# Performance work log

Hardware: AMD Instinct MI355X
Metric: run time of the kernel (lower is better)

Reference implementation:

```python
import jax, jax.numpy as jnp
import numpy as np

N_SITES = 128
BOND = 64
PHYS = 2
BATCH = 8192
EPS = 1e-30


def setup_inputs() -> dict:
    key = jax.random.key(0)
    k0, k1, k2, k3 = jax.random.split(key, 4)
    std = 1.0 / np.sqrt(BOND)  # default init_std in _normal_init
    return {
        "configurations": jax.random.randint(k0, (BATCH, N_SITES), 0, PHYS),
        "left_tensor": jax.random.normal(k1, (1, PHYS, BOND), jnp.float32) * std,
        "bulk_tensors": jax.random.normal(k2, (N_SITES - 2, BOND, PHYS, BOND), jnp.float32) * std,
        "right_tensor": jax.random.normal(k3, (BOND, PHYS, 1), jnp.float32) * std,
    }


def _log_amplitude_squared(left, bulk, right, configs):
    # left: (1,P,D), bulk: (N-2,D,P,D), right: (D,P,1), configs: (B,N) int
    env = left[0, configs[:, 0], :]                         # (B, D)
    m = jnp.clip(jnp.max(jnp.abs(env), axis=1), EPS, None)  # (B,)
    env = env / m[:, None]
    log_scale = jnp.log(m)

    def step(carry, xs):
        env, ls = carry
        A, v = xs                                # A: (D,P,D), v: (B,)
        sel = A[:, v, :]                         # (D, B, D) gathered matrices
        env = jnp.einsum('bi,ibj->bj', env, sel)  # (B, D) batched matvec
        m = jnp.clip(jnp.max(jnp.abs(env), axis=1), EPS, None)
        env = env / m[:, None]
        return (env, ls + jnp.log(m)), None

    (env, log_scale), _ = jax.lax.scan(
        step, (env, log_scale), (bulk, configs[:, 1:-1].T))

    sel = right[:, configs[:, -1], 0]            # (D, B)
    psi = jnp.einsum('bd,db->b', env, sel)       # (B,) rescaled amplitude
    m = jnp.clip(jnp.abs(psi), EPS, None)
    psi = psi / m
    log_scale = log_scale + jnp.log(m)

    abs2 = jnp.clip(psi * psi, EPS, None)
    return jnp.log(abs2) + 2.0 * log_scale      # (B,) log|Psi(v)|^2


def reference(configurations, left_tensor, bulk_tensors, right_tensor):
    return _log_amplitude_squared(left_tensor, bulk_tensors, right_tensor, configurations)
```

## Files before the change

### kernel.cpp

```cpp
#include <hip/hip_runtime.h>
#include <math.h>
#include <stdint.h>

typedef __attribute__((ext_vector_type(8))) short bf16x8;
typedef __attribute__((ext_vector_type(4))) float f32x4;
typedef __attribute__((ext_vector_type(4))) int   i32x4;
typedef __attribute__((ext_vector_type(2))) int   i32x2;

#define NSITES 128
#define NBULK  126
#define BOND   64
#define BATCH  8192

#define WSITE     49152
#define WMASK_OFF ((size_t)NBULK * (size_t)WSITE)
#define WS_NEED   (WMASK_OFF + (size_t)BATCH * 16)

#define EBUF_SZ 12288
#define RED_OFF 24576
#define SMEM_SZ 25088

#define MFMA_BF16 __builtin_amdgcn_mfma_f32_16x16x32_bf16

__global__ void prep_w(const float* __restrict__ bulk, char* __restrict__ wsd) {
    const int s  = blockIdx.x;
    const int t  = threadIdx.x;
    const int jt = (t >> 6) & 3;
    const int l  = t & 63;
    const int j  = jt * 16 + (l & 15);
    const int kb0 = (l >> 4) * 8;
    const float* bs = bulk + (size_t)s * 8192;
    char* dsite = wsd + (size_t)s * WSITE;
    #pragma unroll
    for (int ks = 0; ks < 2; ++ks) {
        const int kb = ks * 32 + kb0;
        #pragma unroll
        for (int v = 0; v < 2; ++v) {
            uint h[3][8];
            #pragma unroll
            for (int e = 0; e < 8; ++e) {
                const float x = bs[(size_t)(kb + e) * 128 + v * 64 + j];
                const uint  u1 = __float_as_uint(x) & 0xffff0000u;
                const float r1 = x - __uint_as_float(u1);
                const uint  u2 = __float_as_uint(r1) & 0xffff0000u;
                const float r2 = r1 - __uint_as_float(u2);
                h[0][e] = u1; h[1][e] = u2;
                h[2][e] = __float_as_uint(r2) & 0xffff0000u;
            }
            #pragma unroll
            for (int tm = 0; tm < 3; ++tm) {
                i32x4 q;
                q.x = (int)((h[tm][0] >> 16) | (h[tm][1] & 0xffff0000u));
                q.y = (int)((h[tm][2] >> 16) | (h[tm][3] & 0xffff0000u));
                q.z = (int)((h[tm][4] >> 16) | (h[tm][5] & 0xffff0000u));
                q.w = (int)((h[tm][6] >> 16) | (h[tm][7] & 0xffff0000u));
                *(i32x4*)(dsite + ((((v*3+tm)*2+ks)*4 + jt) * 1024) + l * 16) = q;
            }
        }
    }
}

__global__ void prep_mask(const int* __restrict__ cfg, uint* __restrict__ msk) {
    const int w = threadIdx.x >> 6, l = threadIdx.x & 63;
    const int b = blockIdx.x * 2 + (w >> 1);
    const int half = w & 1;
    int idx = half * 64 + l + 1;
    if (idx > 127) idx = 127;
    const int v = cfg[b * NSITES + idx];
    const unsigned long long bal = __ballot(v != 0);
    if (l == 0) {
        msk[b * 4 + half * 2]     = (uint)(bal & 0xffffffffu);
        msk[b * 4 + half * 2 + 1] = (uint)(bal >> 32);
    }
}


#define PREFETCH_A(S, DBUF) do { \
    if ((S) < NBULK) { \
        const char* gp_ = ws + (size_t)(S) * WSITE; \
        _Pragma("unroll") for (int vv = 0; vv < 2; ++vv) \
        _Pragma("unroll") for (int tm = 0; tm < 3; ++tm) \
        _Pragma("unroll") for (int ks = 0; ks < 2; ++ks) \
            Areg[DBUF][vv][tm][ks] = *(const bf16x8*)(gp_ + aG[vv][tm][ks]); \
    } \
} while (0)

#define PUBLISH(PW) do { \
    uint pa_[3][4]; \
    _Pragma("unroll") \
    for (int r = 0; r < 4; ++r) { \
        const float x_ = eg0[r]; \
        const uint  u1_ = __float_as_uint(x_) & 0xffff0000u; \
        const float r1_ = x_ - __uint_as_float(u1_); \
        const uint  u2_ = __float_as_uint(r1_) & 0xffff0000u; \
        const float r2_ = r1_ - __uint_as_float(u2_); \
        pa_[0][r] = u1_; pa_[1][r] = u2_; \
        pa_[2][r] = __float_as_uint(r2_) & 0xffff0000u; \
    } \
    _Pragma("unroll") \
    for (int tm = 0; tm < 3; ++tm) { \
        i32x2 d_; \
        d_.x = (int)((pa_[tm][0] >> 16) | (pa_[tm][1] & 0xffff0000u)); \
        d_.y = (int)((pa_[tm][2] >> 16) | (pa_[tm][3] & 0xffff0000u)); \
        *(i32x2*)(smem + aW[PW] + tm * 2048) = d_; \
    } \
    _Pragma("unroll") \
    for (int r = 0; r < 4; ++r) { \
        const float x_ = eg1[r]; \
        const uint  u1_ = __float_as_uint(x_) & 0xffff0000u; \
        const float r1_ = x_ - __uint_as_float(u1_); \
        const uint  u2_ = __float_as_uint(r1_) & 0xffff0000u; \
        const float r2_ = r1_ - __uint_as_float(u2_); \
        pa_[0][r] = u1_; pa_[1][r] = u2_; \
        pa_[2][r] = __float_as_uint(r2_) & 0xffff0000u; \
    } \
    _Pragma("unroll") \
    for (int tm = 0; tm < 3; ++tm) { \
        i32x2 d_; \
        d_.x = (int)((pa_[tm][0] >> 16) | (pa_[tm][1] & 0xffff0000u)); \
        d_.y = (int)((pa_[tm][2] >> 16) | (pa_[tm][3] & 0xffff0000u)); \
        *(i32x2*)(smem + aW[PW] + 6144 + tm * 2048) = d_; \
    } \
} while (0)

#define MSTEP(TW, TE, PAR) \
    _Pragma("unroll") \
    for (int ks = 0; ks < 2; ++ks) { \
        acc00 = MFMA_BF16(Areg[PAR][0][TW][ks], Bf[0][TE][ks], acc00, 0, 0, 0); \
        acc01 = MFMA_BF16(Areg[PAR][1][TW][ks], Bf[0][TE][ks], acc01, 0, 0, 0); \
        acc10 = MFMA_BF16(Areg[PAR][0][TW][ks], Bf[1][TE][ks], acc10, 0, 0, 0); \
        acc11 = MFMA_BF16(Areg[PAR][1][TW][ks], Bf[1][TE][ks], acc11, 0, 0, 0); \
    }

#define SITE_BODY(S, II, PAR, DO_SCALE, DO_MAX) do { \
    PREFETCH_A((S) + 1, (PAR) ^ 1); \
    bf16x8 Bf[2][3][2]; \
    _Pragma("unroll") for (int gg = 0; gg < 2; ++gg) \
    _Pragma("unroll") for (int tm = 0; tm < 3; ++tm) \
    _Pragma("unroll") for (int ks = 0; ks < 2; ++ks) \
        Bf[gg][tm][ks] = *(const bf16x8*)(smem + aB[PAR][ks] + (gg * 3 + tm) * 2048); \
    f32x4 acc00 = {0.f,0.f,0.f,0.f}, acc01 = {0.f,0.f,0.f,0.f}; \
    f32x4 acc10 = {0.f,0.f,0.f,0.f}, acc11 = {0.f,0.f,0.f,0.f}; \
    MSTEP(2,0,PAR) MSTEP(1,1,PAR) MSTEP(0,2,PAR) \
    MSTEP(1,0,PAR) MSTEP(0,1,PAR) MSTEP(0,0,PAR) \
    const bool v0_ = ((mwa >> (II)) & 1u) != 0u; \
    const bool v1_ = ((mwb >> (II)) & 1u) != 0u; \
    eg0.x = v0_ ? acc01.x : acc00.x;  eg0.y = v0_ ? acc01.y : acc00.y; \
    eg0.z = v0_ ? acc01.z : acc00.z;  eg0.w = v0_ ? acc01.w : acc00.w; \
    eg1.x = v1_ ? acc11.x : acc10.x;  eg1.y = v1_ ? acc11.y : acc10.y; \
    eg1.z = v1_ ? acc11.z : acc10.z;  eg1.w = v1_ ? acc11.w : acc10.w; \
    if (DO_SCALE) { \
        f32x4 m4a = *(const f32x4*)(smem + RED_OFF + lb * 16); \
        f32x4 m4b = *(const f32x4*)(smem + RED_OFF + 256 + lb * 16); \
        const float ma = fmaxf(fmaxf(m4a.x, m4a.y), fmaxf(m4a.z, m4a.w)); \
        const float mb = fmaxf(fmaxf(m4b.x, m4b.y), fmaxf(m4b.z, m4b.w)); \
        const int ea = (__float_as_int(ma) >> 23) & 255; \
        const int eb = (__float_as_int(mb) >> 23) & 255; \
        const float sa = __int_as_float((254 - ea) << 23); \
        const float sb = __int_as_float((254 - eb) << 23); \
        ls0 += (float)(ea - 127) * 0.6931471805599453f; \
        ls1 += (float)(eb - 127) * 0.6931471805599453f; \
        eg0.x *= sa; eg0.y *= sa; eg0.z *= sa; eg0.w *= sa; \
        eg1.x *= sb; eg1.y *= sb; eg1.z *= sb; eg1.w *= sb; \
    } \
    if (DO_MAX) { \
        float ma = fmaxf(fmaxf(fabsf(eg0.x), fabsf(eg0.y)), fmaxf(fabsf(eg0.z), fabsf(eg0.w))); \
        float mb = fmaxf(fmaxf(fabsf(eg1.x), fabsf(eg1.y)), fmaxf(fabsf(eg1.z), fabsf(eg1.w))); \
        ma = fmaxf(ma, __shfl_xor(ma, 16)); ma = fmaxf(ma, __shfl_xor(ma, 32)); \
        mb = fmaxf(mb, __shfl_xor(mb, 16)); mb = fmaxf(mb, __shfl_xor(mb, 32)); \
        if (lg == 0) { \
            *(float*)(smem + RED_OFF + lb * 16 + jt * 4) = ma; \
            *(float*)(smem + RED_OFF + 256 + lb * 16 + jt * 4) = mb; \
        } \
    } \
    PUBLISH((PAR) ^ 1); \
    __syncthreads(); \
} while (0)

#define RUN_CHUNK(CB, MWE0, MWE1, CNT, SC0, MXE) { \
    const uint mwa = (MWE0), mwb = (MWE1); \
    _Pragma("unroll 1") \
    for (int i2 = 0; i2 < (CNT); i2 += 2) { \
        SITE_BODY((CB) * 32 + i2,     i2,     0, ((SC0) && i2 == 0),           false); \
        SITE_BODY((CB) * 32 + i2 + 1, i2 + 1, 1, false, ((MXE) && i2 == (CNT) - 2)); \
    } \
}

__global__ __launch_bounds__(256, 1) void mps_main(
    const int*   __restrict__ cfg,
    const float* __restrict__ left,
    const float* __restrict__ right,
    const char*  __restrict__ ws,
    float*       __restrict__ out)
{
    extern __shared__ __align__(16) char smem[];
    const int t  = threadIdx.x;
    const int w  = t >> 6, l = t & 63;
    const int lg = l >> 4, lb = l & 15;
    const int jt = w;
    const int bbase = blockIdx.x * 32;
    const int b0 = bbase + lb, b1 = bbase + 16 + lb;

    int aG[2][3][2];
    #pragma unroll
    for (int vv = 0; vv < 2; ++vv)
        #pragma unroll
        for (int tm = 0; tm < 3; ++tm)
            #pragma unroll
            for (int ks = 0; ks < 2; ++ks)
                aG[vv][tm][ks] = (((vv*3+tm)*2 + ks)*4 + jt) * 1024 + l * 16;

    int aB[2][2], aW[2];
    {
        const int key = lb & 7;
        const int s0 = ((0 + lg) ^ key) * 16;
        const int s1 = ((4 + lg) ^ key) * 16;
        aB[0][0] = lb * 128 + s0;          aB[0][1] = lb * 128 + s1;
        aB[1][0] = aB[0][0] + EBUF_SZ;     aB[1][1] = aB[0][1] + EBUF_SZ;
        aW[0] = lb * 128 + (((jt * 2 + (lg >> 1)) ^ key) * 16) + (lg & 1) * 8;
        aW[1] = aW[0] + EBUF_SZ;
    }

    bf16x8 Areg[2][2][3][2];
    float ls0 = 0.f, ls1 = 0.f;
    f32x4 eg0 = {0.f,0.f,0.f,0.f}, eg1 = {0.f,0.f,0.f,0.f};

    PREFETCH_A(0, 0);

    const uint* mp = (const uint*)(ws + WMASK_OFF);
    uint4 vmg0 = *(const uint4*)(mp + (size_t)b0 * 4);
    uint4 vmg1 = *(const uint4*)(mp + (size_t)b1 * 4);
    const int c00 = cfg[b0 * NSITES], c01 = cfg[b1 * NSITES];
    const int jout = jt * 16 + lg * 4;
    #pragma unroll
    for (int r = 0; r < 4; ++r) {
        eg0[r] = left[c00 * BOND + jout + r];
        eg1[r] = left[c01 * BOND + jout + r];
    }
    PUBLISH(0);
    __syncthreads();

    RUN_CHUNK(0, vmg0.x, vmg1.x, 32, false, true)
    RUN_CHUNK(1, vmg0.y, vmg1.y, 32, true,  true)
    RUN_CHUNK(2, vmg0.z, vmg1.z, 32, true,  true)
    RUN_CHUNK(3, vmg0.w, vmg1.w, 30, true,  false)

    {
        const int vl0 = cfg[b0 * NSITES + 127], vl1 = cfg[b1 * NSITES + 127];
        float p0 = eg0.x * right[(jout + 0) * 2 + vl0] + eg0.y * right[(jout + 1) * 2 + vl0]
                 + eg0.z * right[(jout + 2) * 2 + vl0] + eg0.w * right[(jout + 3) * 2 + vl0];
        float p1 = eg1.x * right[(jout + 0) * 2 + vl1] + eg1.y * right[(jout + 1) * 2 + vl1]
                 + eg1.z * right[(jout + 2) * 2 + vl1] + eg1.w * right[(jout + 3) * 2 + vl1];
        p0 += __shfl_xor(p0, 16); p0 += __shfl_xor(p0, 32);
        p1 += __shfl_xor(p1, 16); p1 += __shfl_xor(p1, 32);
        if (lg == 0) {
            *(float*)(smem + RED_OFF + lb * 16 + jt * 4) = p0;
            *(float*)(smem + RED_OFF + 256 + lb * 16 + jt * 4) = p1;
        }
    }
    __syncthreads();
    if (w == 0 && l < 16) {
        f32x4 q0 = *(const f32x4*)(smem + RED_OFF + lb * 16);
        f32x4 q1 = *(const f32x4*)(smem + RED_OFF + 256 + lb * 16);
        const float s0 = (q0.x + q0.y) + (q0.z + q0.w);
        const float s1 = (q1.x + q1.y) + (q1.z + q1.w);
        out[b0] = 2.0f * (ls0 + logf(fmaxf(fabsf(s0), 1e-30f)));
        out[b1] = 2.0f * (ls1 + logf(fmaxf(fabsf(s1), 1e-30f)));
    }
}

#define WPB     16
#define TPB     (WPB * 64)
#define SITE_ELTS (BOND * 2 * BOND)

__global__ __launch_bounds__(TPB, 2) void mps_logamp_fp32(
    const int*   __restrict__ cfg, const float* __restrict__ left,
    const float* __restrict__ bulk, const float* __restrict__ right,
    float* __restrict__ out)
{
    __shared__ float Abuf[2][SITE_ELTS];
    __shared__ float envs[WPB][BOND];
    __shared__ int   cfgs[WPB * NSITES];
    const int t = threadIdx.x;
    const int w = t >> 6, l = t & 63;
    const int bbase = blockIdx.x * WPB;
    const int b = bbase + w;
    cfgs[t] = cfg[bbase * NSITES + t];
    cfgs[t + TPB] = cfg[bbase * NSITES + t + TPB];
    { const float4* src = (const float4*)bulk; float4* dst = (float4*)(&Abuf[0][0]);
      dst[t] = src[t]; dst[t + TPB] = src[t + TPB]; }
    __syncthreads();
    const int c0 = cfgs[w * NSITES];
    float e = left[c0 * BOND + l];
    float m = fabsf(e);
    #pragma unroll
    for (int k = 32; k; k >>= 1) m = fmaxf(m, __shfl_xor(m, k));
    m = fmaxf(m, 1e-30f);
    e = e / m;
    float ls = logf(m);
    envs[w][l] = e;
    for (int s = 0; s < NBULK; ++s) {
        const int cur = s & 1, nxt = cur ^ 1;
        const bool pf = (s + 1 < NBULK);
        float4 p0, p1;
        if (pf) { const float4* src = (const float4*)(bulk + (size_t)(s + 1) * SITE_ELTS);
                  p0 = src[t]; p1 = src[t + TPB]; }
        const int v = cfgs[w * NSITES + (s + 1)];
        const float* Ap = &Abuf[cur][v * BOND + l];
        const float* ev = &envs[w][0];
        float acc = 0.0f;
        #pragma unroll
        for (int i = 0; i < BOND; i += 4) {
            const float4 e4 = *(const float4*)(ev + i);
            acc = fmaf(e4.x, Ap[(i + 0) * 128], acc);
            acc = fmaf(e4.y, Ap[(i + 1) * 128], acc);
            acc = fmaf(e4.z, Ap[(i + 2) * 128], acc);
            acc = fmaf(e4.w, Ap[(i + 3) * 128], acc);
        }
        float mm = fabsf(acc);
        #pragma unroll
        for (int k = 32; k; k >>= 1) mm = fmaxf(mm, __shfl_xor(mm, k));
        mm = fmaxf(mm, 1e-30f);
        acc = acc / mm;
        ls += logf(mm);
        if (pf) { float4* dst = (float4*)(&Abuf[nxt][0]); dst[t] = p0; dst[t + TPB] = p1; }
        envs[w][l] = acc;
        e = acc;
        __syncthreads();
    }
    const int vl = cfgs[w * NSITES + (NSITES - 1)];
    float p = e * right[l * 2 + vl];
    #pragma unroll
    for (int k = 32; k; k >>= 1) p += __shfl_xor(p, k);
    const float am = fmaxf(fabsf(p), 1e-30f);
    if (l == 0) out[b] = 2.0f * (ls + logf(am));
}

extern "C" void kernel_launch(void* const* d_in, const int* in_sizes, int n_in,
                              void* d_out, int out_size, void* d_ws, size_t ws_size,
                              hipStream_t stream) {
    const int*   cfg   = (const int*)d_in[0];
    const float* left  = (const float*)d_in[1];
    const float* bulk  = (const float*)d_in[2];
    const float* right = (const float*)d_in[3];
    float*       out   = (float*)d_out;

    if (ws_size >= WS_NEED) {
        hipLaunchKernelGGL(prep_w, dim3(NBULK), dim3(256), 0, stream,
                           bulk, (char*)d_ws);
        hipLaunchKernelGGL(prep_mask, dim3(BATCH / 2), dim3(256), 0, stream,
                           cfg, (uint*)((char*)d_ws + WMASK_OFF));
        hipLaunchKernelGGL(mps_main, dim3(BATCH / 32), dim3(256), SMEM_SZ, stream,
                           cfg, left, right, (const char*)d_ws, out);
    } else {
        hipLaunchKernelGGL(mps_logamp_fp32, dim3(BATCH / WPB), dim3(TPB), 0, stream,
                           cfg, left, bulk, right, out);
    }
}
```

Measured before the change: 125.6 us.

## Halve batch rows per block to double grid size and allow two blocks per CU

Each workgroup of mps_main now handles 16 configurations instead of 32. The grid goes from 256 to 512 blocks, shared memory per block shrinks by half, and launch bounds now allow two blocks per CU. The aim is to fill more of the device (256 blocks do not cover all CUs) and to hide the serial per-site latency of the MFMA and barrier chain. In exchange, each weight fragment streamed from global memory into registers is reused across half as many batch rows, which doubles total weight traffic.

```diff
diff --git a/kernel.cpp b/kernel.cpp
--- a/kernel.cpp
+++ b/kernel.cpp
@@ -16,9 +16,9 @@
 #define WMASK_OFF ((size_t)NBULK * (size_t)WSITE)
 #define WS_NEED   (WMASK_OFF + (size_t)BATCH * 16)
 
-#define EBUF_SZ 12288
-#define RED_OFF 24576
-#define SMEM_SZ 25088
+#define EBUF_SZ 6144
+#define RED_OFF 12288
+#define SMEM_SZ 12800
 
 #define MFMA_BF16 __builtin_amdgcn_mfma_f32_16x16x32_bf16
 
@@ -104,81 +104,46 @@
         d_.y = (int)((pa_[tm][2] >> 16) | (pa_[tm][3] & 0xffff0000u)); \
         *(i32x2*)(smem + aW[PW] + tm * 2048) = d_; \
     } \
-    _Pragma("unroll") \
-    for (int r = 0; r < 4; ++r) { \
-        const float x_ = eg1[r]; \
-        const uint  u1_ = __float_as_uint(x_) & 0xffff0000u; \
-        const float r1_ = x_ - __uint_as_float(u1_); \
-        const uint  u2_ = __float_as_uint(r1_) & 0xffff0000u; \
-        const float r2_ = r1_ - __uint_as_float(u2_); \
-        pa_[0][r] = u1_; pa_[1][r] = u2_; \
-        pa_[2][r] = __float_as_uint(r2_) & 0xffff0000u; \
-    } \
-    _Pragma("unroll") \
-    for (int tm = 0; tm < 3; ++tm) { \
-        i32x2 d_; \
-        d_.x = (int)((pa_[tm][0] >> 16) | (pa_[tm][1] & 0xffff0000u)); \
-        d_.y = (int)((pa_[tm][2] >> 16) | (pa_[tm][3] & 0xffff0000u)); \
-        *(i32x2*)(smem + aW[PW] + 6144 + tm * 2048) = d_; \
-    } \
 } while (0)
 
 #define MSTEP(TW, TE, PAR) \
     _Pragma("unroll") \
     for (int ks = 0; ks < 2; ++ks) { \
-        acc00 = MFMA_BF16(Areg[PAR][0][TW][ks], Bf[0][TE][ks], acc00, 0, 0, 0); \
-        acc01 = MFMA_BF16(Areg[PAR][1][TW][ks], Bf[0][TE][ks], acc01, 0, 0, 0); \
-        acc10 = MFMA_BF16(Areg[PAR][0][TW][ks], Bf[1][TE][ks], acc10, 0, 0, 0); \
-        acc11 = MFMA_BF16(Areg[PAR][1][TW][ks], Bf[1][TE][ks], acc11, 0, 0, 0); \
+        acc00 = MFMA_BF16(Areg[PAR][0][TW][ks], Bf[TE][ks], acc00, 0, 0, 0); \
+        acc01 = MFMA_BF16(Areg[PAR][1][TW][ks], Bf[TE][ks], acc01, 0, 0, 0); \
     }
 
 #define SITE_BODY(S, II, PAR, DO_SCALE, DO_MAX) do { \
     PREFETCH_A((S) + 1, (PAR) ^ 1); \
-    bf16x8 Bf[2][3][2]; \
-    _Pragma("unroll") for (int gg = 0; gg < 2; ++gg) \
+    bf16x8 Bf[3][2]; \
     _Pragma("unroll") for (int tm = 0; tm < 3; ++tm) \
     _Pragma("unroll") for (int ks = 0; ks < 2; ++ks) \
-        Bf[gg][tm][ks] = *(const bf16x8*)(smem + aB[PAR][ks] + (gg * 3 + tm) * 2048); \
+        Bf[tm][ks] = *(const bf16x8*)(smem + aB[PAR][ks] + tm * 2048); \
     f32x4 acc00 = {0.f,0.f,0.f,0.f}, acc01 = {0.f,0.f,0.f,0.f}; \
-    f32x4 acc10 = {0.f,0.f,0.f,0.f}, acc11 = {0.f,0.f,0.f,0.f}; \
     MSTEP(2,0,PAR) MSTEP(1,1,PAR) MSTEP(0,2,PAR) \
     MSTEP(1,0,PAR) MSTEP(0,1,PAR) MSTEP(0,0,PAR) \
     const bool v0_ = ((mwa >> (II)) & 1u) != 0u; \
-    const bool v1_ = ((mwb >> (II)) & 1u) != 0u; \
     eg0.x = v0_ ? acc01.x : acc00.x;  eg0.y = v0_ ? acc01.y : acc00.y; \
     eg0.z = v0_ ? acc01.z : acc00.z;  eg0.w = v0_ ? acc01.w : acc00.w; \
-    eg1.x = v1_ ? acc11.x : acc10.x;  eg1.y = v1_ ? acc11.y : acc10.y; \
-    eg1.z = v1_ ? acc11.z : acc10.z;  eg1.w = v1_ ? acc11.w : acc10.w; \
     if (DO_SCALE) { \
         f32x4 m4a = *(const f32x4*)(smem + RED_OFF + lb * 16); \
-        f32x4 m4b = *(const f32x4*)(smem + RED_OFF + 256 + lb * 16); \
         const float ma = fmaxf(fmaxf(m4a.x, m4a.y), fmaxf(m4a.z, m4a.w)); \
-        const float mb = fmaxf(fmaxf(m4b.x, m4b.y), fmaxf(m4b.z, m4b.w)); \
         const int ea = (__float_as_int(ma) >> 23) & 255; \
-        const int eb = (__float_as_int(mb) >> 23) & 255; \
         const float sa = __int_as_float((254 - ea) << 23); \
-        const float sb = __int_as_float((254 - eb) << 23); \
         ls0 += (float)(ea - 127) * 0.6931471805599453f; \
-        ls1 += (float)(eb - 127) * 0.6931471805599453f; \
         eg0.x *= sa; eg0.y *= sa; eg0.z *= sa; eg0.w *= sa; \
-        eg1.x *= sb; eg1.y *= sb; eg1.z *= sb; eg1.w *= sb; \
     } \
     if (DO_MAX) { \
         float ma = fmaxf(fmaxf(fabsf(eg0.x), fabsf(eg0.y)), fmaxf(fabsf(eg0.z), fabsf(eg0.w))); \
-        float mb = fmaxf(fmaxf(fabsf(eg1.x), fabsf(eg1.y)), fmaxf(fabsf(eg1.z), fabsf(eg1.w))); \
         ma = fmaxf(ma, __shfl_xor(ma, 16)); ma = fmaxf(ma, __shfl_xor(ma, 32)); \
-        mb = fmaxf(mb, __shfl_xor(mb, 16)); mb = fmaxf(mb, __shfl_xor(mb, 32)); \
-        if (lg == 0) { \
-            *(float*)(smem + RED_OFF + lb * 16 + jt * 4) = ma; \
-            *(float*)(smem + RED_OFF + 256 + lb * 16 + jt * 4) = mb; \
-        } \
+        if (lg == 0) *(float*)(smem + RED_OFF + lb * 16 + jt * 4) = ma; \
     } \
     PUBLISH((PAR) ^ 1); \
     __syncthreads(); \
 } while (0)
 
-#define RUN_CHUNK(CB, MWE0, MWE1, CNT, SC0, MXE) { \
-    const uint mwa = (MWE0), mwb = (MWE1); \
+#define RUN_CHUNK(CB, MWE0, CNT, SC0, MXE) { \
+    const uint mwa = (MWE0); \
     _Pragma("unroll 1") \
     for (int i2 = 0; i2 < (CNT); i2 += 2) { \
         SITE_BODY((CB) * 32 + i2,     i2,     0, ((SC0) && i2 == 0),           false); \
@@ -186,7 +151,7 @@
     } \
 }
 
-__global__ __launch_bounds__(256, 1) void mps_main(
+__global__ __launch_bounds__(256, 2) void mps_main(
     const int*   __restrict__ cfg,
     const float* __restrict__ left,
     const float* __restrict__ right,
@@ -198,8 +163,7 @@
     const int w  = t >> 6, l = t & 63;
     const int lg = l >> 4, lb = l & 15;
     const int jt = w;
-    const int bbase = blockIdx.x * 32;
-    const int b0 = bbase + lb, b1 = bbase + 16 + lb;
+    const int b0 = blockIdx.x * 16 + lb;
 
     int aG[2][3][2];
     #pragma unroll
@@ -222,50 +186,37 @@
     }
 
     bf16x8 Areg[2][2][3][2];
-    float ls0 = 0.f, ls1 = 0.f;
-    f32x4 eg0 = {0.f,0.f,0.f,0.f}, eg1 = {0.f,0.f,0.f,0.f};
+    float ls0 = 0.f;
+    f32x4 eg0 = {0.f,0.f,0.f,0.f};
 
     PREFETCH_A(0, 0);
 
     const uint* mp = (const uint*)(ws + WMASK_OFF);
     uint4 vmg0 = *(const uint4*)(mp + (size_t)b0 * 4);
-    uint4 vmg1 = *(const uint4*)(mp + (size_t)b1 * 4);
-    const int c00 = cfg[b0 * NSITES], c01 = cfg[b1 * NSITES];
+    const int c00 = cfg[b0 * NSITES];
     const int jout = jt * 16 + lg * 4;
     #pragma unroll
-    for (int r = 0; r < 4; ++r) {
-        eg0[r] = left[c00 * BOND + jout + r];
-        eg1[r] = left[c01 * BOND + jout + r];
-    }
+    for (int r = 0; r < 4; ++r) eg0[r] = left[c00 * BOND + jout + r];
     PUBLISH(0);
     __syncthreads();
 
-    RUN_CHUNK(0, vmg0.x, vmg1.x, 32, false, true)
-    RUN_CHUNK(1, vmg0.y, vmg1.y, 32, true,  true)
-    RUN_CHUNK(2, vmg0.z, vmg1.z, 32, true,  true)
-    RUN_CHUNK(3, vmg0.w, vmg1.w, 30, true,  false)
+    RUN_CHUNK(0, vmg0.x, 32, false, true)
+    RUN_CHUNK(1, vmg0.y, 32, true,  true)
+    RUN_CHUNK(2, vmg0.z, 32, true,  true)
+    RUN_CHUNK(3, vmg0.w, 30, true,  false)
 
     {
-        const int vl0 = cfg[b0 * NSITES + 127], vl1 = cfg[b1 * NSITES + 127];
+        const int vl0 = cfg[b0 * NSITES + 127];
         float p0 = eg0.x * right[(jout + 0) * 2 + vl0] + eg0.y * right[(jout + 1) * 2 + vl0]
                  + eg0.z * right[(jout + 2) * 2 + vl0] + eg0.w * right[(jout + 3) * 2 + vl0];
-        float p1 = eg1.x * right[(jout + 0) * 2 + vl1] + eg1.y * right[(jout + 1) * 2 + vl1]
-                 + eg1.z * right[(jout + 2) * 2 + vl1] + eg1.w * right[(jout + 3) * 2 + vl1];
         p0 += __shfl_xor(p0, 16); p0 += __shfl_xor(p0, 32);
-        p1 += __shfl_xor(p1, 16); p1 += __shfl_xor(p1, 32);
-        if (lg == 0) {
-            *(float*)(smem + RED_OFF + lb * 16 + jt * 4) = p0;
-            *(float*)(smem + RED_OFF + 256 + lb * 16 + jt * 4) = p1;
-        }
+        if (lg == 0) *(float*)(smem + RED_OFF + lb * 16 + jt * 4) = p0;
     }
     __syncthreads();
     if (w == 0 && l < 16) {
         f32x4 q0 = *(const f32x4*)(smem + RED_OFF + lb * 16);
-        f32x4 q1 = *(const f32x4*)(smem + RED_OFF + 256 + lb * 16);
         const float s0 = (q0.x + q0.y) + (q0.z + q0.w);
-        const float s1 = (q1.x + q1.y) + (q1.z + q1.w);
         out[b0] = 2.0f * (ls0 + logf(fmaxf(fabsf(s0), 1e-30f)));
-        out[b1] = 2.0f * (ls1 + logf(fmaxf(fabsf(s1), 1e-30f)));
     }
 }
 
@@ -350,7 +301,7 @@
                            bulk, (char*)d_ws);
         hipLaunchKernelGGL(prep_mask, dim3(BATCH / 2), dim3(256), 0, stream,
                            cfg, (uint*)((char*)d_ws + WMASK_OFF));
-        hipLaunchKernelGGL(mps_main, dim3(BATCH / 32), dim3(256), SMEM_SZ, stream,
+        hipLaunchKernelGGL(mps_main, dim3(BATCH / 16), dim3(256), SMEM_SZ, stream,
                            cfg, left, right, (const char*)d_ws, out);
     } else {
         hipLaunchKernelGGL(mps_logamp_fp32, dim3(BATCH / WPB), dim3(TPB), 0, stream,
```

Result: slower. 136.8 us (+8.9%).
